# Optimization experiments

Measured on AMD Instinct MI355X. Metric: run time of the kernel, lower is better.

The kernel has to match this reference:

```python
import jax, jax.numpy as jnp
import numpy as np

MODEL_DIM = 1024
TOTAL_DIM = 1024
N_HEADS = 16
HEAD_DIM = TOTAL_DIM // N_HEADS


def setup_inputs() -> dict:
    key = jax.random.key(0)
    k1, k2, k3 = jax.random.split(key, 3)
    query = jax.random.normal(k1, (2, 2048, MODEL_DIM), dtype=jnp.float32)
    # nn.Linear(model_dim, 3*total_dim, bias=False): store as [in, out] for x @ W
    W_in = jax.random.normal(k2, (MODEL_DIM, 3 * TOTAL_DIM), dtype=jnp.float32) / np.sqrt(MODEL_DIM)
    W_out = jax.random.normal(k3, (TOTAL_DIM, MODEL_DIM), dtype=jnp.float32) / np.sqrt(TOTAL_DIM)
    return {"query": query, "W_in": W_in, "W_out": W_out}


def reference(query, W_in, W_out):
    B, S, _ = query.shape
    qkv = query @ W_in                      # [B, S, 3*D]
    q, k, v = jnp.split(qkv, 3, axis=-1)    # each [B, S, D]

    def to_heads(t):
        return t.reshape(B, S, N_HEADS, HEAD_DIM).transpose(0, 2, 1, 3)  # [B,H,S,d]

    q, k, v = to_heads(q), to_heads(k), to_heads(v)
    scale = 1.0 / np.sqrt(HEAD_DIM).astype(np.float32)
    scores = jnp.einsum('bhqd,bhkd->bhqk', q, k) * scale  # [B,H,S,S]
    causal = jnp.tril(jnp.ones((S, S), dtype=bool))
    scores = jnp.where(causal, scores, jnp.finfo(scores.dtype).min)
    probs = jax.nn.softmax(scores, axis=-1)
    attn = jnp.einsum('bhqk,bhkd->bhqd', probs, v)        # [B,H,S,d]
    attn = attn.transpose(0, 2, 1, 3).reshape(B, S, TOTAL_DIM)
    return attn @ W_out                     # [B, S, model_dim]
```

## Files before the change

kernel.cpp:

```cpp
#include <hip/hip_runtime.h>


typedef __bf16 bf16x8 __attribute__((ext_vector_type(8)));
typedef float f32x4 __attribute__((ext_vector_type(4)));
typedef int i32x4 __attribute__((ext_vector_type(4)));

#define B_   2
#define S_   2048
#define DM   1024
#define NH   16
#define HD   64
#define N3   3072
#define M_   4096

#define SCALE_LOG2E 0.180336884f

__device__ __forceinline__ unsigned short f2bf(float f) {
  unsigned int u = __float_as_uint(f);
  u += 0x7fffu + ((u >> 16) & 1u);
  return (unsigned short)(u >> 16);
}

__device__ __forceinline__ void gload_lds16(void* lds, const void* g) {
  __builtin_amdgcn_global_load_lds(
      (__attribute__((address_space(1))) void*)g,
      (__attribute__((address_space(3))) void*)lds, 16, 0, 0);
}

__global__ __launch_bounds__(256) void f32_to_bf16_vec(
    const float4* __restrict__ in, unsigned short* __restrict__ out, int n4) {
  int i = blockIdx.x * 256 + threadIdx.x;
  if (i < n4) {
    float4 v = in[i];
    ushort4 o;
    o.x = f2bf(v.x); o.y = f2bf(v.y); o.z = f2bf(v.z); o.w = f2bf(v.w);
    *(ushort4*)(&out[(size_t)i * 4]) = o;
  }
}

__global__ __launch_bounds__(256) void transpose_f32_bf16(
    const float* __restrict__ in, unsigned short* __restrict__ out, int R, int C,
    int scale_rows, float scale) {
  __shared__ float tile[32][33];
  const int tx = threadIdx.x, ty = threadIdx.y;
  const int x = blockIdx.x * 32 + tx;
  const int y0 = blockIdx.y * 32;
#pragma unroll
  for (int j = 0; j < 32; j += 8)
    tile[ty + j][tx] = in[(size_t)(y0 + ty + j) * C + x];
  __syncthreads();
  const int ox = y0 + tx;
  const int oy0 = blockIdx.x * 32;
#pragma unroll
  for (int j = 0; j < 32; j += 8) {
    const int orow = oy0 + ty + j;
    float v = tile[tx][ty + j];
    if (orow < scale_rows) v *= scale;
    out[(size_t)orow * R + ox] = f2bf(v);
  }
}

__global__ __launch_bounds__(256) void transpose_v(
    const unsigned short* __restrict__ qkv, unsigned short* __restrict__ vT) {
  __shared__ unsigned short tile[32][33];
  const int tx = threadIdx.x, ty = threadIdx.y;
  const int c0 = blockIdx.x * 32;
  const int r0 = blockIdx.y * 32;
#pragma unroll
  for (int j = 0; j < 32; j += 8)
    tile[ty + j][tx] = qkv[(size_t)(r0 + ty + j) * N3 + 2 * DM + c0 + tx];
  __syncthreads();
  const int b = r0 >> 11;
  const int srow = (r0 & 2047);
  const int head = c0 >> 6;
#pragma unroll
  for (int j = 0; j < 32; j += 8) {
    const int d = (c0 & 63) + ty + j;
    vT[(size_t)((b * NH + head) * HD + d) * S_ + srow + tx] = tile[tx][ty + j];
  }
}

template <int OUT_BF16>
__global__ __launch_bounds__(256) void gemm_abt(
    const unsigned short* __restrict__ A, const unsigned short* __restrict__ Bt,
    void* __restrict__ Cv, int M, int N, int K) {
  __shared__ __align__(16) unsigned short a_sm[128 * 32];
  __shared__ __align__(16) unsigned short b_sm[128 * 32];
  const int tid = threadIdx.x;
  const int lane = tid & 63, wave = tid >> 6;
  const int quad = lane >> 4, l15 = lane & 15;
  const int row0 = blockIdx.y * 128, col0 = blockIdx.x * 128;
  const int wm = (wave >> 1) * 64, wn = (wave & 1) * 64;

  f32x4 acc[4][4];
#pragma unroll
  for (int i = 0; i < 4; i++)
#pragma unroll
    for (int j = 0; j < 4; j++) acc[i][j] = (f32x4){0.f, 0.f, 0.f, 0.f};

  const int e0 = tid * 8;

  for (int k0 = 0; k0 < K; k0 += 32) {
    __syncthreads();
#pragma unroll
    for (int i = 0; i < 2; i++) {
      int e = e0 + i * 2048;
      int r = e >> 5, c = e & 31;
      gload_lds16(&a_sm[e], &A[(size_t)(row0 + r) * K + k0 + c]);
      gload_lds16(&b_sm[e], &Bt[(size_t)(col0 + r) * K + k0 + c]);
    }
    __syncthreads();

    bf16x8 af[4], bfb[4];
#pragma unroll
    for (int i = 0; i < 4; i++) {
      af[i]  = *(const bf16x8*)&a_sm[(wm + i * 16 + l15) * 32 + quad * 8];
      bfb[i] = *(const bf16x8*)&b_sm[(wn + i * 16 + l15) * 32 + quad * 8];
    }
#pragma unroll
    for (int i = 0; i < 4; i++)
#pragma unroll
      for (int j = 0; j < 4; j++)
        acc[i][j] = __builtin_amdgcn_mfma_f32_16x16x32_bf16(af[i], bfb[j], acc[i][j], 0, 0, 0);
  }

#pragma unroll
  for (int i = 0; i < 4; i++) {
#pragma unroll
    for (int j = 0; j < 4; j++) {
#pragma unroll
      for (int r = 0; r < 4; r++) {
        const int row = row0 + wm + i * 16 + quad * 4 + r;
        const int col = col0 + wn + j * 16 + l15;
        const float v = acc[i][j][r];
        if (OUT_BF16)
          ((unsigned short*)Cv)[(size_t)row * N + col] = f2bf(v);
        else
          ((float*)Cv)[(size_t)row * N + col] = v;
      }
    }
  }
}

__global__ __launch_bounds__(512, 4) void attn_fused9(
    const unsigned short* __restrict__ qkv,
    const unsigned short* __restrict__ vT,
    unsigned short* __restrict__ attnout) {
  const int h = blockIdx.y, b = blockIdx.z;
  const int j = blockIdx.x;
  const int tid = threadIdx.x;
  const int lane = tid & 63, wave = tid >> 6;
  const int quad = lane >> 4, l15 = lane & 15;
  const int sw = l15 & 7;

  __shared__ __align__(16) unsigned short k_sm[4 * 4096];
  __shared__ __align__(16) unsigned short vt_sm[4 * 4096];

  const int wrow0 = (wave < 4) ? (j * 64 + wave * 16)
                               : ((31 - j) * 64 + (wave - 4) * 16);
  const int qrow = wrow0 + l15;

  bf16x8 qf[2];
  {
    const unsigned short* qp = qkv + (size_t)(b * S_ + qrow) * N3 + h * HD + quad * 8;
    qf[0] = *(const bf16x8*)qp;
    qf[1] = *(const bf16x8*)(qp + 32);
  }

  f32x4 o[4];
#pragma unroll
  for (int n = 0; n < 4; n++) o[n] = (f32x4){0.f, 0.f, 0.f, 0.f};
  float lsum = 0.f;

  const int r0s = tid >> 3;
  const int gch = ((tid & 7) ^ (r0s & 7)) * 8;
  const unsigned short* kgb = qkv + (size_t)(b * S_ + r0s) * N3 + DM + h * HD + gch;
  const unsigned short* vgb = vT + (size_t)((b * NH + h) * HD + r0s) * S_ + gch;

  const int addrA = (((quad * 2) & 3) * 16 + l15) * 4;
  const int addrB = (((quad * 2 + 1) & 3) * 16 + l15) * 4;

  const int nt = 32 - j;

  int pk[4][2];
  const unsigned short* vbp = &vt_sm[0];
  const bool hi = quad >= 2;

  auto PV = [&]() {
#pragma unroll
    for (int ks = 0; ks < 2; ks++) {
      const int m0 = 2 * ks, m1 = m0 + 1;
      const int f0a = __builtin_amdgcn_ds_bpermute(addrA, pk[m0][0]);
      const int f0b = __builtin_amdgcn_ds_bpermute(addrA, pk[m1][0]);
      const int f1a = __builtin_amdgcn_ds_bpermute(addrA, pk[m0][1]);
      const int f1b = __builtin_amdgcn_ds_bpermute(addrA, pk[m1][1]);
      const int f2a = __builtin_amdgcn_ds_bpermute(addrB, pk[m0][0]);
      const int f2b = __builtin_amdgcn_ds_bpermute(addrB, pk[m1][0]);
      const int f3a = __builtin_amdgcn_ds_bpermute(addrB, pk[m0][1]);
      const int f3b = __builtin_amdgcn_ds_bpermute(addrB, pk[m1][1]);
      i32x4 fr;
      fr.x = hi ? f0b : f0a;
      fr.y = hi ? f1b : f1a;
      fr.z = hi ? f2b : f2a;
      fr.w = hi ? f3b : f3a;
      const bf16x8 pfrag = __builtin_bit_cast(bf16x8, fr);
#pragma unroll
      for (int mb = 0; mb < 4; mb++) {
        const int ro = (mb * 16 + l15) * 64;
        bf16x8 vf = *(const bf16x8*)&vbp[ro + (((ks * 4 + quad) ^ sw) << 3)];
        o[mb] = __builtin_amdgcn_mfma_f32_16x16x32_bf16(vf, pfrag, o[mb], 0, 0, 0);
      }
    }
  };

  gload_lds16(&k_sm[tid * 8], kgb);
  gload_lds16(&vt_sm[tid * 8], vgb);
  gload_lds16(&k_sm[4096 + tid * 8], kgb + (size_t)64 * N3);
  gload_lds16(&vt_sm[4096 + tid * 8], vgb + 64);

  for (int t = 0; t < nt; t++) {
    if (t + 1 < nt) asm volatile("s_waitcnt vmcnt(2)" ::: "memory");
    else            asm volatile("s_waitcnt vmcnt(0)" ::: "memory");
    __builtin_amdgcn_s_barrier();
    __builtin_amdgcn_sched_barrier(0);
    if (t + 2 < nt) {
      const int b2 = (t + 2) & 3;
      gload_lds16(&k_sm[b2 * 4096 + tid * 8], kgb + (size_t)(t + 2) * 64 * N3);
      gload_lds16(&vt_sm[b2 * 4096 + tid * 8], vgb + (t + 2) * 64);
    }
    const unsigned short* kb = &k_sm[(t & 3) * 4096];
    const unsigned short* vb = &vt_sm[(t & 3) * 4096];

    if (t >= 1 && (t - 1) * 64 <= wrow0 + 15) PV();

    if (t * 64 <= wrow0 + 15) {
      f32x4 s[4];
#pragma unroll
      for (int mb = 0; mb < 4; mb++) s[mb] = (f32x4){0.f, 0.f, 0.f, 0.f};
#pragma unroll
      for (int mb = 0; mb < 4; mb++) {
        const int ro = (mb * 16 + l15) * 64;
        bf16x8 kf0 = *(const bf16x8*)&kb[ro + ((quad ^ sw) << 3)];
        bf16x8 kf1 = *(const bf16x8*)&kb[ro + (((4 + quad) ^ sw) << 3)];
        s[mb] = __builtin_amdgcn_mfma_f32_16x16x32_bf16(kf0, qf[0], s[mb], 0, 0, 0);
        s[mb] = __builtin_amdgcn_mfma_f32_16x16x32_bf16(kf1, qf[1], s[mb], 0, 0, 0);
      }

      if (t * 64 + 63 <= wrow0) {
#pragma unroll
        for (int mb = 0; mb < 4; mb++)
#pragma unroll
          for (int r = 0; r < 4; r++)
            s[mb][r] = exp2f(s[mb][r]);
      } else {
        const int kq0 = t * 64 + quad * 4;
#pragma unroll
        for (int mb = 0; mb < 4; mb++)
#pragma unroll
          for (int r = 0; r < 4; r++) {
            const float e = exp2f(s[mb][r]);
            s[mb][r] = (kq0 + mb * 16 + r <= qrow) ? e : 0.f;
          }
      }
#pragma unroll
      for (int mb = 0; mb < 4; mb++)
        lsum += (s[mb][0] + s[mb][1]) + (s[mb][2] + s[mb][3]);

#pragma unroll
      for (int mb = 0; mb < 4; mb++) {
        const unsigned u0 = __float_as_uint(s[mb][0]) + 0x8000u;
        const unsigned u1 = __float_as_uint(s[mb][1]) + 0x8000u;
        const unsigned u2 = __float_as_uint(s[mb][2]) + 0x8000u;
        const unsigned u3 = __float_as_uint(s[mb][3]) + 0x8000u;
        pk[mb][0] = (int)__builtin_amdgcn_perm(u1, u0, 0x07060302u);
        pk[mb][1] = (int)__builtin_amdgcn_perm(u3, u2, 0x07060302u);
      }
      vbp = vb;
    }
  }

  if ((nt - 1) * 64 <= wrow0 + 15) PV();

  asm volatile("s_waitcnt vmcnt(0)" ::: "memory");

  float l = lsum;
  l += __shfl_xor(l, 16);
  l += __shfl_xor(l, 32);
  const float inv = 1.0f / l;
  const size_t grow = (size_t)(b * S_ + qrow);
#pragma unroll
  for (int mb = 0; mb < 4; mb++) {
    ushort4 w;
    w.x = f2bf(o[mb][0] * inv);
    w.y = f2bf(o[mb][1] * inv);
    w.z = f2bf(o[mb][2] * inv);
    w.w = f2bf(o[mb][3] * inv);
    *(ushort4*)&attnout[grow * DM + h * HD + mb * 16 + quad * 4] = w;
  }
}

extern "C" void kernel_launch(void* const* d_in, const int* in_sizes, int n_in,
                              void* d_out, int out_size, void* d_ws, size_t ws_size,
                              hipStream_t stream) {
  const float* query = (const float*)d_in[0];
  const float* w_in  = (const float*)d_in[1];
  const float* w_out = (const float*)d_in[2];
  float* out = (float*)d_out;

  char* ws = (char*)d_ws;
  unsigned short* qbf     = (unsigned short*)(ws);
  unsigned short* vT      = (unsigned short*)(ws);
  unsigned short* w_in_t  = (unsigned short*)(ws + 8388608);
  unsigned short* w_out_t = (unsigned short*)(ws + 14680064);
  unsigned short* qkv     = (unsigned short*)(ws + 16777216);
  unsigned short* attn    = (unsigned short*)(ws + 41943040);

  f32_to_bf16_vec<<<dim3(M_ * DM / 1024), dim3(256), 0, stream>>>(
      (const float4*)query, qbf, M_ * DM / 4);
  transpose_f32_bf16<<<dim3(N3 / 32, DM / 32), dim3(32, 8), 0, stream>>>(
      w_in, w_in_t, DM, N3, DM, SCALE_LOG2E);
  transpose_f32_bf16<<<dim3(DM / 32, DM / 32), dim3(32, 8), 0, stream>>>(
      w_out, w_out_t, DM, DM, 0, 1.0f);
  gemm_abt<1><<<dim3(N3 / 128, M_ / 128), dim3(256), 0, stream>>>(qbf, w_in_t, qkv, M_, N3, DM);
  transpose_v<<<dim3(DM / 32, M_ / 32), dim3(32, 8), 0, stream>>>(qkv, vT);
  attn_fused9<<<dim3(16, NH, B_), dim3(512), 0, stream>>>(qkv, vT, attn);
  gemm_abt<0><<<dim3(DM / 128, M_ / 128), dim3(256), 0, stream>>>(attn, w_out_t, out, M_, DM, DM);
}
```

Measured before the change: 204.1 us.

## Process paired causal query tiles sequentially in 256-thread attention blocks

The attention kernel drops from 512 threads, where two wave groups handled the query tiles j and 31-j at the same time, to 256 threads. Each block now walks tile A and then tile 31-A in one continuous 33-step key loop, flushing and reloading Q at the switch. This removes the idle waves from the short-tile half and keeps every wave busy through a balanced loop. The cost is half the parallelism per block and a longer serial loop. Each stage also loads twice as many chunks per thread, and the wait counts were changed to match.

```diff
diff --git a/kernel.cpp b/kernel.cpp
--- a/kernel.cpp
+++ b/kernel.cpp
@@ -142,12 +142,12 @@
   }
 }
 
-__global__ __launch_bounds__(512, 4) void attn_fused9(
+__global__ __launch_bounds__(256, 2) void attn_fused10(
     const unsigned short* __restrict__ qkv,
     const unsigned short* __restrict__ vT,
     unsigned short* __restrict__ attnout) {
   const int h = blockIdx.y, b = blockIdx.z;
-  const int j = blockIdx.x;
+  const int A = blockIdx.x;
   const int tid = threadIdx.x;
   const int lane = tid & 63, wave = tid >> 6;
   const int quad = lane >> 4, l15 = lane & 15;
@@ -156,9 +156,11 @@
   __shared__ __align__(16) unsigned short k_sm[4 * 4096];
   __shared__ __align__(16) unsigned short vt_sm[4 * 4096];
 
-  const int wrow0 = (wave < 4) ? (j * 64 + wave * 16)
-                               : ((31 - j) * 64 + (wave - 4) * 16);
-  const int qrow = wrow0 + l15;
+  const int ntA = A + 1;
+  const int NT = 33;
+
+  int qt = A;
+  int qrow = qt * 64 + wave * 16 + l15;
 
   bf16x8 qf[2];
   {
@@ -180,7 +182,15 @@
   const int addrA = (((quad * 2) & 3) * 16 + l15) * 4;
   const int addrB = (((quad * 2 + 1) & 3) * 16 + l15) * 4;
 
-  const int nt = 32 - j;
+  auto STAGE = [&](int w, int buf) {
+    const int ktw = (w < ntA) ? w : (w - ntA);
+    const unsigned short* kgt = kgb + (size_t)ktw * 64 * N3;
+    const unsigned short* vgt = vgb + ktw * 64;
+    gload_lds16(&k_sm[buf * 4096 + tid * 8], kgt);
+    gload_lds16(&k_sm[buf * 4096 + tid * 8 + 2048], kgt + (size_t)32 * N3);
+    gload_lds16(&vt_sm[buf * 4096 + tid * 8], vgt);
+    gload_lds16(&vt_sm[buf * 4096 + tid * 8 + 2048], vgt + (size_t)32 * S_);
+  };
 
   int pk[4][2];
   const unsigned short* vbp = &vt_sm[0];
@@ -213,90 +223,98 @@
     }
   };
 
-  gload_lds16(&k_sm[tid * 8], kgb);
-  gload_lds16(&vt_sm[tid * 8], vgb);
-  gload_lds16(&k_sm[4096 + tid * 8], kgb + (size_t)64 * N3);
-  gload_lds16(&vt_sm[4096 + tid * 8], vgb + 64);
-
-  for (int t = 0; t < nt; t++) {
-    if (t + 1 < nt) asm volatile("s_waitcnt vmcnt(2)" ::: "memory");
+  auto FLUSH = [&](int qr) {
+    float l = lsum;
+    l += __shfl_xor(l, 16);
+    l += __shfl_xor(l, 32);
+    const float inv = 1.0f / l;
+    const size_t grow = (size_t)(b * S_ + qr);
+#pragma unroll
+    for (int mb = 0; mb < 4; mb++) {
+      ushort4 w;
+      w.x = f2bf(o[mb][0] * inv);
+      w.y = f2bf(o[mb][1] * inv);
+      w.z = f2bf(o[mb][2] * inv);
+      w.w = f2bf(o[mb][3] * inv);
+      *(ushort4*)&attnout[grow * DM + h * HD + mb * 16 + quad * 4] = w;
+    }
+  };
+
+  STAGE(0, 0);
+  STAGE(1, 1);
+
+  for (int t = 0; t < NT; t++) {
+    if (t + 1 < NT) asm volatile("s_waitcnt vmcnt(4)" ::: "memory");
     else            asm volatile("s_waitcnt vmcnt(0)" ::: "memory");
     __builtin_amdgcn_s_barrier();
     __builtin_amdgcn_sched_barrier(0);
-    if (t + 2 < nt) {
-      const int b2 = (t + 2) & 3;
-      gload_lds16(&k_sm[b2 * 4096 + tid * 8], kgb + (size_t)(t + 2) * 64 * N3);
-      gload_lds16(&vt_sm[b2 * 4096 + tid * 8], vgb + (t + 2) * 64);
-    }
+    if (t + 2 < NT) STAGE(t + 2, (t + 2) & 3);
+
     const unsigned short* kb = &k_sm[(t & 3) * 4096];
     const unsigned short* vb = &vt_sm[(t & 3) * 4096];
 
-    if (t >= 1 && (t - 1) * 64 <= wrow0 + 15) PV();
-
-    if (t * 64 <= wrow0 + 15) {
-      f32x4 s[4];
-#pragma unroll
-      for (int mb = 0; mb < 4; mb++) s[mb] = (f32x4){0.f, 0.f, 0.f, 0.f};
-#pragma unroll
-      for (int mb = 0; mb < 4; mb++) {
-        const int ro = (mb * 16 + l15) * 64;
-        bf16x8 kf0 = *(const bf16x8*)&kb[ro + ((quad ^ sw) << 3)];
-        bf16x8 kf1 = *(const bf16x8*)&kb[ro + (((4 + quad) ^ sw) << 3)];
-        s[mb] = __builtin_amdgcn_mfma_f32_16x16x32_bf16(kf0, qf[0], s[mb], 0, 0, 0);
-        s[mb] = __builtin_amdgcn_mfma_f32_16x16x32_bf16(kf1, qf[1], s[mb], 0, 0, 0);
-      }
-
-      if (t * 64 + 63 <= wrow0) {
-#pragma unroll
-        for (int mb = 0; mb < 4; mb++)
-#pragma unroll
-          for (int r = 0; r < 4; r++)
-            s[mb][r] = exp2f(s[mb][r]);
-      } else {
-        const int kq0 = t * 64 + quad * 4;
-#pragma unroll
-        for (int mb = 0; mb < 4; mb++)
-#pragma unroll
-          for (int r = 0; r < 4; r++) {
-            const float e = exp2f(s[mb][r]);
-            s[mb][r] = (kq0 + mb * 16 + r <= qrow) ? e : 0.f;
-          }
-      }
+    if (t >= 1) PV();
+
+    if (t == ntA) {
+      FLUSH(qrow);
+#pragma unroll
+      for (int n = 0; n < 4; n++) o[n] = (f32x4){0.f, 0.f, 0.f, 0.f};
+      lsum = 0.f;
+      qt = 31 - A;
+      qrow = qt * 64 + wave * 16 + l15;
+      const unsigned short* qp = qkv + (size_t)(b * S_ + qrow) * N3 + h * HD + quad * 8;
+      qf[0] = *(const bf16x8*)qp;
+      qf[1] = *(const bf16x8*)(qp + 32);
+    }
+
+    const int kt = (t < ntA) ? t : (t - ntA);
+    f32x4 s[4];
+#pragma unroll
+    for (int mb = 0; mb < 4; mb++) s[mb] = (f32x4){0.f, 0.f, 0.f, 0.f};
+#pragma unroll
+    for (int mb = 0; mb < 4; mb++) {
+      const int ro = (mb * 16 + l15) * 64;
+      bf16x8 kf0 = *(const bf16x8*)&kb[ro + ((quad ^ sw) << 3)];
+      bf16x8 kf1 = *(const bf16x8*)&kb[ro + (((4 + quad) ^ sw) << 3)];
+      s[mb] = __builtin_amdgcn_mfma_f32_16x16x32_bf16(kf0, qf[0], s[mb], 0, 0, 0);
+      s[mb] = __builtin_amdgcn_mfma_f32_16x16x32_bf16(kf1, qf[1], s[mb], 0, 0, 0);
+    }
+
+    if (kt != qt) {
 #pragma unroll
       for (int mb = 0; mb < 4; mb++)
-        lsum += (s[mb][0] + s[mb][1]) + (s[mb][2] + s[mb][3]);
-
-#pragma unroll
-      for (int mb = 0; mb < 4; mb++) {
-        const unsigned u0 = __float_as_uint(s[mb][0]) + 0x8000u;
-        const unsigned u1 = __float_as_uint(s[mb][1]) + 0x8000u;
-        const unsigned u2 = __float_as_uint(s[mb][2]) + 0x8000u;
-        const unsigned u3 = __float_as_uint(s[mb][3]) + 0x8000u;
-        pk[mb][0] = (int)__builtin_amdgcn_perm(u1, u0, 0x07060302u);
-        pk[mb][1] = (int)__builtin_amdgcn_perm(u3, u2, 0x07060302u);
-      }
-      vbp = vb;
-    }
-  }
-
-  if ((nt - 1) * 64 <= wrow0 + 15) PV();
-
+#pragma unroll
+        for (int r = 0; r < 4; r++)
+          s[mb][r] = exp2f(s[mb][r]);
+    } else {
+      const int kq0 = kt * 64 + quad * 4;
+#pragma unroll
+      for (int mb = 0; mb < 4; mb++)
+#pragma unroll
+        for (int r = 0; r < 4; r++) {
+          const float e = exp2f(s[mb][r]);
+          s[mb][r] = (kq0 + mb * 16 + r <= qrow) ? e : 0.f;
+        }
+    }
+#pragma unroll
+    for (int mb = 0; mb < 4; mb++)
+      lsum += (s[mb][0] + s[mb][1]) + (s[mb][2] + s[mb][3]);
+
+#pragma unroll
+    for (int mb = 0; mb < 4; mb++) {
+      const unsigned u0 = __float_as_uint(s[mb][0]) + 0x8000u;
+      const unsigned u1 = __float_as_uint(s[mb][1]) + 0x8000u;
+      const unsigned u2 = __float_as_uint(s[mb][2]) + 0x8000u;
+      const unsigned u3 = __float_as_uint(s[mb][3]) + 0x8000u;
+      pk[mb][0] = (int)__builtin_amdgcn_perm(u1, u0, 0x07060302u);
+      pk[mb][1] = (int)__builtin_amdgcn_perm(u3, u2, 0x07060302u);
+    }
+    vbp = vb;
+  }
+
+  PV();
   asm volatile("s_waitcnt vmcnt(0)" ::: "memory");
-
-  float l = lsum;
-  l += __shfl_xor(l, 16);
-  l += __shfl_xor(l, 32);
-  const float inv = 1.0f / l;
-  const size_t grow = (size_t)(b * S_ + qrow);
-#pragma unroll
-  for (int mb = 0; mb < 4; mb++) {
-    ushort4 w;
-    w.x = f2bf(o[mb][0] * inv);
-    w.y = f2bf(o[mb][1] * inv);
-    w.z = f2bf(o[mb][2] * inv);
-    w.w = f2bf(o[mb][3] * inv);
-    *(ushort4*)&attnout[grow * DM + h * HD + mb * 16 + quad * 4] = w;
-  }
+  FLUSH(qrow);
 }
 
 extern "C" void kernel_launch(void* const* d_in, const int* in_sizes, int n_in,
@@ -323,6 +341,6 @@
       w_out, w_out_t, DM, DM, 0, 1.0f);
   gemm_abt<1><<<dim3(N3 / 128, M_ / 128), dim3(256), 0, stream>>>(qbf, w_in_t, qkv, M_, N3, DM);
   transpose_v<<<dim3(DM / 32, M_ / 32), dim3(32, 8), 0, stream>>>(qkv, vT);
-  attn_fused9<<<dim3(16, NH, B_), dim3(512), 0, stream>>>(qkv, vT, attn);
+  attn_fused10<<<dim3(16, NH, B_), dim3(256), 0, stream>>>(qkv, vT, attn);
   gemm_abt<0><<<dim3(DM / 128, M_ / 128), dim3(256), 0, stream>>>(attn, w_out_t, out, M_, DM, DM);
 }
```

New measurement: 205.7 us. About the same (+0.8%).

## Pre-swizzle V into MFMA fragment order to drop bpermute shuffles in PV

Applied to the files above, without the earlier changes.

The V transpose kernel now writes V in a tile-blocked layout that already matches the MFMA operand order, one contiguous 4096-element block per 64-key tile. The attention kernel loads those blocks with plain contiguous copies. PV then runs two 16x16x16 MFMAs per block, taking the probability registers straight from the S accumulators, so the eight ds_bpermute cross-lane shuffles per step are gone. The cost is twice as many smaller MFMAs, plus LDS reads in the new V layout that may hit bank conflicts.

```diff
diff --git a/kernel.cpp b/kernel.cpp
--- a/kernel.cpp
+++ b/kernel.cpp
@@ -2,8 +2,10 @@
 
 
 typedef __bf16 bf16x8 __attribute__((ext_vector_type(8)));
+typedef __bf16 bf16x4 __attribute__((ext_vector_type(4)));
+typedef short s16x4 __attribute__((ext_vector_type(4)));
 typedef float f32x4 __attribute__((ext_vector_type(4)));
-typedef int i32x4 __attribute__((ext_vector_type(4)));
+typedef int i32x2 __attribute__((ext_vector_type(2)));
 
 #define B_   2
 #define S_   2048
@@ -25,6 +27,15 @@
   __builtin_amdgcn_global_load_lds(
       (__attribute__((address_space(1))) void*)g,
       (__attribute__((address_space(3))) void*)lds, 16, 0, 0);
+}
+
+__device__ __forceinline__ f32x4 mfma16(bf16x4 a, bf16x4 b, f32x4 c) {
+#if __has_builtin(__builtin_amdgcn_mfma_f32_16x16x16_bf16)
+  return __builtin_amdgcn_mfma_f32_16x16x16_bf16(a, b, c, 0, 0, 0);
+#else
+  return __builtin_amdgcn_mfma_f32_16x16x16bf16_1k(
+      __builtin_bit_cast(s16x4, a), __builtin_bit_cast(s16x4, b), c, 0, 0, 0);
+#endif
 }
 
 __global__ __launch_bounds__(256) void f32_to_bf16_vec(
@@ -61,22 +72,34 @@
 }
 
 __global__ __launch_bounds__(256) void transpose_v(
-    const unsigned short* __restrict__ qkv, unsigned short* __restrict__ vT) {
-  __shared__ unsigned short tile[32][33];
-  const int tx = threadIdx.x, ty = threadIdx.y;
-  const int c0 = blockIdx.x * 32;
-  const int r0 = blockIdx.y * 32;
-#pragma unroll
-  for (int j = 0; j < 32; j += 8)
-    tile[ty + j][tx] = qkv[(size_t)(r0 + ty + j) * N3 + 2 * DM + c0 + tx];
+    const unsigned short* __restrict__ qkv, unsigned short* __restrict__ vTn) {
+  __shared__ unsigned short tile[64][72];
+  const int kt = blockIdx.x;
+  const int h  = blockIdx.y;
+  const int b  = blockIdx.z;
+  const int t  = threadIdx.x;
+  const int row = t >> 3;
+  const int c8  = (t & 7) * 8;
+#pragma unroll
+  for (int rr = 0; rr < 2; rr++) {
+    const int s = row + rr * 32;
+    const size_t src = (size_t)(b * S_ + kt * 64 + s) * N3 + 2 * DM + h * HD + c8;
+    *(float4*)&tile[s][c8] = *(const float4*)&qkv[src];
+  }
   __syncthreads();
-  const int b = r0 >> 11;
-  const int srow = (r0 & 2047);
-  const int head = c0 >> 6;
-#pragma unroll
-  for (int j = 0; j < 32; j += 8) {
-    const int d = (c0 & 63) + ty + j;
-    vT[(size_t)((b * NH + head) * HD + d) * S_ + srow + tx] = tile[tx][ty + j];
+  const size_t base = (size_t)((b * NH + h) * 32 + kt) * 4096;
+#pragma unroll
+  for (int u0 = 0; u0 < 2; u0++) {
+    const int u = t + u0 * 256;
+    const int p = u >> 8, d = (u >> 2) & 63, q = u & 3;
+    const int s0 = 32 * p + q * 4;
+    ushort4 w0, w1;
+    w0.x = tile[s0 + 0][d];  w0.y = tile[s0 + 1][d];
+    w0.z = tile[s0 + 2][d];  w0.w = tile[s0 + 3][d];
+    w1.x = tile[s0 + 16][d]; w1.y = tile[s0 + 17][d];
+    w1.z = tile[s0 + 18][d]; w1.w = tile[s0 + 19][d];
+    *(ushort4*)&vTn[base + (size_t)u * 8]     = w0;
+    *(ushort4*)&vTn[base + (size_t)u * 8 + 4] = w1;
   }
 }
 
@@ -142,9 +165,9 @@
   }
 }
 
-__global__ __launch_bounds__(512, 4) void attn_fused9(
+__global__ __launch_bounds__(512, 4) void attn_fused11(
     const unsigned short* __restrict__ qkv,
-    const unsigned short* __restrict__ vT,
+    const unsigned short* __restrict__ vTn,
     unsigned short* __restrict__ attnout) {
   const int h = blockIdx.y, b = blockIdx.z;
   const int j = blockIdx.x;
@@ -175,48 +198,38 @@
   const int r0s = tid >> 3;
   const int gch = ((tid & 7) ^ (r0s & 7)) * 8;
   const unsigned short* kgb = qkv + (size_t)(b * S_ + r0s) * N3 + DM + h * HD + gch;
-  const unsigned short* vgb = vT + (size_t)((b * NH + h) * HD + r0s) * S_ + gch;
-
-  const int addrA = (((quad * 2) & 3) * 16 + l15) * 4;
-  const int addrB = (((quad * 2 + 1) & 3) * 16 + l15) * 4;
+  const unsigned short* vgl = vTn + (size_t)((b * NH + h) * 32) * 4096 + tid * 8;
 
   const int nt = 32 - j;
 
   int pk[4][2];
   const unsigned short* vbp = &vt_sm[0];
-  const bool hi = quad >= 2;
 
   auto PV = [&]() {
 #pragma unroll
-    for (int ks = 0; ks < 2; ks++) {
-      const int m0 = 2 * ks, m1 = m0 + 1;
-      const int f0a = __builtin_amdgcn_ds_bpermute(addrA, pk[m0][0]);
-      const int f0b = __builtin_amdgcn_ds_bpermute(addrA, pk[m1][0]);
-      const int f1a = __builtin_amdgcn_ds_bpermute(addrA, pk[m0][1]);
-      const int f1b = __builtin_amdgcn_ds_bpermute(addrA, pk[m1][1]);
-      const int f2a = __builtin_amdgcn_ds_bpermute(addrB, pk[m0][0]);
-      const int f2b = __builtin_amdgcn_ds_bpermute(addrB, pk[m1][0]);
-      const int f3a = __builtin_amdgcn_ds_bpermute(addrB, pk[m0][1]);
-      const int f3b = __builtin_amdgcn_ds_bpermute(addrB, pk[m1][1]);
-      i32x4 fr;
-      fr.x = hi ? f0b : f0a;
-      fr.y = hi ? f1b : f1a;
-      fr.z = hi ? f2b : f2a;
-      fr.w = hi ? f3b : f3a;
-      const bf16x8 pfrag = __builtin_bit_cast(bf16x8, fr);
+    for (int p = 0; p < 2; p++) {
+      i32x2 wlo, whi;
+      wlo.x = pk[2 * p][0];     wlo.y = pk[2 * p][1];
+      whi.x = pk[2 * p + 1][0]; whi.y = pk[2 * p + 1][1];
+      const bf16x4 blo = __builtin_bit_cast(bf16x4, wlo);
+      const bf16x4 bhi = __builtin_bit_cast(bf16x4, whi);
 #pragma unroll
       for (int mb = 0; mb < 4; mb++) {
-        const int ro = (mb * 16 + l15) * 64;
-        bf16x8 vf = *(const bf16x8*)&vbp[ro + (((ks * 4 + quad) ^ sw) << 3)];
-        o[mb] = __builtin_amdgcn_mfma_f32_16x16x32_bf16(vf, pfrag, o[mb], 0, 0, 0);
+        const bf16x8 vv =
+            *(const bf16x8*)&vbp[(p * 256 + mb * 64 + l15 * 4 + quad) * 8];
+        bf16x4 alo, ahi;
+#pragma unroll
+        for (int i = 0; i < 4; i++) { alo[i] = vv[i]; ahi[i] = vv[i + 4]; }
+        o[mb] = mfma16(alo, blo, o[mb]);
+        o[mb] = mfma16(ahi, bhi, o[mb]);
       }
     }
   };
 
   gload_lds16(&k_sm[tid * 8], kgb);
-  gload_lds16(&vt_sm[tid * 8], vgb);
+  gload_lds16(&vt_sm[tid * 8], vgl);
   gload_lds16(&k_sm[4096 + tid * 8], kgb + (size_t)64 * N3);
-  gload_lds16(&vt_sm[4096 + tid * 8], vgb + 64);
+  gload_lds16(&vt_sm[4096 + tid * 8], vgl + 4096);
 
   for (int t = 0; t < nt; t++) {
     if (t + 1 < nt) asm volatile("s_waitcnt vmcnt(2)" ::: "memory");
@@ -226,7 +239,7 @@
     if (t + 2 < nt) {
       const int b2 = (t + 2) & 3;
       gload_lds16(&k_sm[b2 * 4096 + tid * 8], kgb + (size_t)(t + 2) * 64 * N3);
-      gload_lds16(&vt_sm[b2 * 4096 + tid * 8], vgb + (t + 2) * 64);
+      gload_lds16(&vt_sm[b2 * 4096 + tid * 8], vgl + (size_t)(t + 2) * 4096);
     }
     const unsigned short* kb = &k_sm[(t & 3) * 4096];
     const unsigned short* vb = &vt_sm[(t & 3) * 4096];
@@ -309,7 +322,7 @@
 
   char* ws = (char*)d_ws;
   unsigned short* qbf     = (unsigned short*)(ws);
-  unsigned short* vT      = (unsigned short*)(ws);
+  unsigned short* vTn     = (unsigned short*)(ws);
   unsigned short* w_in_t  = (unsigned short*)(ws + 8388608);
   unsigned short* w_out_t = (unsigned short*)(ws + 14680064);
   unsigned short* qkv     = (unsigned short*)(ws + 16777216);
@@ -322,7 +335,7 @@
   transpose_f32_bf16<<<dim3(DM / 32, DM / 32), dim3(32, 8), 0, stream>>>(
       w_out, w_out_t, DM, DM, 0, 1.0f);
   gemm_abt<1><<<dim3(N3 / 128, M_ / 128), dim3(256), 0, stream>>>(qbf, w_in_t, qkv, M_, N3, DM);
-  transpose_v<<<dim3(DM / 32, M_ / 32), dim3(32, 8), 0, stream>>>(qkv, vT);
-  attn_fused9<<<dim3(16, NH, B_), dim3(512), 0, stream>>>(qkv, vT, attn);
+  transpose_v<<<dim3(32, NH, B_), dim3(256), 0, stream>>>(qkv, vTn);
+  attn_fused11<<<dim3(16, NH, B_), dim3(512), 0, stream>>>(qkv, vTn, attn);
   gemm_abt<0><<<dim3(DM / 128, M_ / 128), dim3(256), 0, stream>>>(attn, w_out_t, out, M_, DM, DM);
 }
```

After: 198.8 us. 1.03x faster.
